# Optimization experiments

Hardware: AMD Instinct MI355X
Metric: run time of the kernel (lower is better)

Reference implementation:

```python
import jax, jax.numpy as jnp
import numpy as np

G, B, N, D = 3, 4096, 32, 256
C, H, A, L = 128, 8, 128, 16


def setup_inputs() -> dict:
    key = jax.random.key(0)
    ks = jax.random.split(key, 9)
    return {
        "targets": jax.random.normal(ks[0], (B, D), jnp.float32),
        "contexts": jax.random.normal(ks[1], (G, B, N, D), jnp.float32),
        "kernel": jax.random.normal(ks[2], (D, C), jnp.float32) * 0.05,
        "attn_kernel": jax.random.normal(ks[3], (1, H, 2 * C), jnp.float32) * 0.05,
        "attn_bias": jnp.zeros((H * C,), jnp.float32),
        "sem_kernel": jax.random.normal(ks[4], (H * C, A), jnp.float32) * 0.05,
        "sem_att_kernel": jax.random.normal(ks[5], (A, 1), jnp.float32) * 0.05,
        "dense_w": jax.random.normal(ks[6], (H * C, L), jnp.float32) * 0.05,
        "dense_b": jnp.zeros((L,), jnp.float32),
    }


def reference(targets, contexts, kernel, attn_kernel, attn_bias, sem_kernel,
              sem_att_kernel, dense_w, dense_b):
    # NodeAttention (shared weights across metapath groups; vectorized over G)
    node = jnp.einsum('bd,dc->bc', targets, kernel)            # [B,C]
    neigh = jnp.einsum('gbnd,dc->gbnc', contexts, kernel)      # [G,B,N,C]
    g, b, n, c = neigh.shape
    ak = attn_kernel[0]                                        # [H,2C]
    ak_node, ak_neigh = ak[:, :c], ak[:, c:]                   # split of concat([node, neigh])
    # scores[g,b,n,h] = concat(node_b, neigh_gbn) . ak_h
    scores = (jnp.einsum('bc,hc->bh', node, ak_node)[None, :, None, :]
              + jnp.einsum('gbnc,hc->gbnh', neigh, ak_neigh))  # [G,B,N,H]
    scores = jnp.transpose(scores, (0, 1, 3, 2))               # [G,B,H,N]
    coef = jax.nn.softmax(jax.nn.leaky_relu(scores, 0.2), axis=-1)
    z = jnp.einsum('gbhn,gbnc->gbhc', coef, neigh)             # [G,B,H,C]
    z = z.reshape(g, b, -1) + attn_bias                        # [G,B,H*C] (concat=True)
    # SemanticAttention over metapath groups
    inp = jnp.transpose(z, (1, 0, 2))                          # [B,G,HC]
    s = jnp.squeeze(jnp.matmul(jnp.tanh(jnp.matmul(inp, sem_kernel)), sem_att_kernel), -1)  # [B,G]
    att = jax.nn.softmax(s, axis=-1)
    pooled = jnp.einsum('bg,bgd->bd', att, inp)                # [B,HC]
    logits = pooled @ dense_w + dense_b                        # [B,L]
    return logits
```

## Files before the change

kernel.cpp:

```cpp
#include <hip/hip_runtime.h>
#include <hip/hip_bf16.h>

typedef float v4f __attribute__((ext_vector_type(4)));
typedef short v8s __attribute__((ext_vector_type(8)));

__device__ __forceinline__ unsigned short f2bf(float x){
    unsigned u = __float_as_uint(x);
    u += 0x7FFFu + ((u >> 16) & 1u);
    return (unsigned short)(u >> 16);
}
__device__ __forceinline__ float bf2f(unsigned short h){
    return __uint_as_float(((unsigned)h) << 16);
}
__device__ __forceinline__ v8s pack_bf8(v4f a, v4f b){
    union { v8s s; __hip_bfloat162 h[4]; } u;
    u.h[0] = __float22bfloat162_rn(float2{a[0],a[1]});
    u.h[1] = __float22bfloat162_rn(float2{a[2],a[3]});
    u.h[2] = __float22bfloat162_rn(float2{b[0],b[1]});
    u.h[3] = __float22bfloat162_rn(float2{b[2],b[3]});
    return u.s;
}

__global__ __launch_bounds__(256) void prep_all(const float* __restrict__ targ,
        const float* __restrict__ kern, const float* __restrict__ ak,
        const float* __restrict__ semk, float* __restrict__ ns,
        unsigned short* __restrict__ packB, unsigned short* __restrict__ pack2){
    __shared__ float wsh[256*8];
    int blk = blockIdx.x, t = threadIdx.x;
    if (blk < 16){
        {
            float a[8];
            #pragma unroll
            for (int h=0;h<8;h++) a[h]=0.f;
            const float* kr = kern + t*128;
            for (int c=0;c<128;c++){
                float kv = kr[c];
                #pragma unroll
                for (int h=0;h<8;h++) a[h] = fmaf(kv, ak[h*256+c], a[h]);
            }
            #pragma unroll
            for (int h=0;h<8;h++) wsh[t*8+h]=a[h];
        }
        __syncthreads();
        int b = blk*256 + t;
        float acc[8];
        #pragma unroll
        for (int h=0;h<8;h++) acc[h]=0.f;
        const float* tr = targ + (size_t)b*256;
        for (int d=0;d<256;d++){
            float tv = tr[d];
            #pragma unroll
            for (int h=0;h<8;h++) acc[h] = fmaf(tv, wsh[d*8+h], acc[h]);
        }
        #pragma unroll
        for (int h=0;h<8;h++) ns[b*8+h]=acc[h];
    } else if (blk < 18){
        {
            float a[8];
            #pragma unroll
            for (int h=0;h<8;h++) a[h]=0.f;
            const float* kr = kern + t*128;
            for (int c=0;c<128;c++){
                float kv = kr[c];
                #pragma unroll
                for (int h=0;h<8;h++) a[h] = fmaf(kv, ak[h*256+128+c], a[h]);
            }
            #pragma unroll
            for (int h=0;h<8;h++) wsh[t*8+h]=a[h];
        }
        __syncthreads();
        int gt = (blk-16)*256 + t;
        for (int r=0;r<72;r++){
            int e = gt + r*512;
            int j = e & 7; int l = (e>>3) & 63;
            int fc = e >> 9; int cc = fc % 9; int kk = fc / 9;
            int d = kk*32 + (l>>4)*8 + j;
            int c = cc*16 + (l&15);
            float v;
            if (cc < 8) v = kern[d*128 + c];
            else { int h = c - 128; v = (h < 8) ? wsh[d*8+h] : 0.0f; }
            packB[e] = f2bf(v);
        }
    } else {
        int gt = (blk-18)*256 + t;
        for (int r=0;r<16;r++){
            int e = gt + r*8192;
            int j = e & 7; int l = (e>>3) & 63;
            int cc = (e>>9) & 7; int gkk = e >> 12;
            int k = gkk*32 + (l>>4)*8 + j;
            int a2 = cc*16 + (l&15);
            pack2[e] = f2bf(semk[k*128 + a2]);
        }
    }
}

__global__ __launch_bounds__(256,4) void phase1(const float* __restrict__ ctx,
        const unsigned short* __restrict__ packB, const float* __restrict__ ns,
        const float* __restrict__ bias, unsigned short* __restrict__ zb16){
    __shared__ __align__(16) unsigned short outT[64*146];
    __shared__ float cf[2*32*8];

    int t = threadIdx.x;
    int bid = blockIdx.x;
    int g  = bid >> 11;
    int b0 = (bid & 2047) * 2;
    int w = t >> 6, lane = t & 63;

    const float* abase = ctx + (size_t)((g*4096 + b0)*32 + w*16 + (lane&15))*256 + ((lane>>4)*8);
    const unsigned short* bbase = packB + lane*8;

    v4f acc[9];
    #pragma unroll
    for (int i=0;i<9;i++) acc[i] = (v4f){0.f,0.f,0.f,0.f};

    #pragma unroll
    for (int kk=0;kk<8;kk++){
        v4f a0 = *(const v4f*)(abase + kk*32);
        v4f a1 = *(const v4f*)(abase + kk*32 + 4);
        v8s afr = pack_bf8(a0, a1);
        #pragma unroll
        for (int cc=0;cc<9;cc++){
            v8s bfr = *(const v8s*)(bbase + (kk*9+cc)*512);
            acc[cc] = __builtin_amdgcn_mfma_f32_16x16x32_bf16(afr, bfr, acc[cc], 0,0,0);
        }
    }

    int qr = (lane>>4)*4;
    #pragma unroll
    for (int cc=0;cc<9;cc++){
        int col = cc*16 + (lane&15);
        #pragma unroll
        for (int r=0;r<4;r++)
            outT[(w*16 + qr + r)*146 + col] = f2bf(acc[cc][r]);
    }
    __syncthreads();

    {
        int p = t >> 4, i = t & 15;
        int b = p >> 3, h = p & 7;
        float nsv = ns[(b0 + b)*8 + h];
        int row0 = b*32 + i, row1 = row0 + 16;
        float s0 = bf2f(outT[row0*146 + 128 + h]) + nsv;
        float s1 = bf2f(outT[row1*146 + 128 + h]) + nsv;
        s0 = s0 > 0.f ? s0 : 0.2f*s0;
        s1 = s1 > 0.f ? s1 : 0.2f*s1;
        float m = fmaxf(s0, s1);
        #pragma unroll
        for (int d=1; d<16; d<<=1) m = fmaxf(m, __shfl_xor(m, d));
        float e0 = __expf(s0 - m), e1 = __expf(s1 - m);
        float ssum = e0 + e1;
        #pragma unroll
        for (int d=1; d<16; d<<=1) ssum += __shfl_xor(ssum, d);
        float inv = 1.0f / ssum;
        cf[(b*32 + i)*8 + h]      = e0 * inv;
        cf[(b*32 + i + 16)*8 + h] = e1 * inv;
    }
    __syncthreads();

    {
        int b = t >> 7, c = t & 127;
        float az[8];
        #pragma unroll
        for (int h=0;h<8;h++) az[h]=0.f;
        for (int n=0;n<32;n++){
            float v = bf2f(outT[(b*32+n)*146 + c]);
            v4f c0 = *(const v4f*)&cf[(b*32+n)*8];
            v4f c1 = *(const v4f*)&cf[(b*32+n)*8 + 4];
            az[0] = fmaf(c0[0], v, az[0]); az[1] = fmaf(c0[1], v, az[1]);
            az[2] = fmaf(c0[2], v, az[2]); az[3] = fmaf(c0[3], v, az[3]);
            az[4] = fmaf(c1[0], v, az[4]); az[5] = fmaf(c1[1], v, az[5]);
            az[6] = fmaf(c1[2], v, az[6]); az[7] = fmaf(c1[3], v, az[7]);
        }
        size_t zb = ((size_t)(b0 + b)*3 + g)*1024;
        #pragma unroll
        for (int h=0;h<8;h++) zb16[zb + h*128 + c] = f2bf(az[h] + bias[h*128 + c]);
    }
}

__global__ __launch_bounds__(256) void semk2(const unsigned short* __restrict__ zb16,
        const unsigned short* __restrict__ pack2, const float* __restrict__ sa,
        float* __restrict__ sws){
    __shared__ float red[16*4];
    int t = threadIdx.x, w = t>>6, lane = t&63;
    int r0 = blockIdx.x * 16;
    v4f acc0 = (v4f){0.f,0.f,0.f,0.f};
    v4f acc1 = (v4f){0.f,0.f,0.f,0.f};
    const unsigned short* abase = zb16 + (size_t)(r0 + (lane&15))*1024 + (lane>>4)*8;
    #pragma unroll 4
    for (int kk=0; kk<32; kk++){
        v8s afr = *(const v8s*)(abase + kk*32);
        v8s b0  = *(const v8s*)(pack2 + (((kk*8 + w  )*64 + lane) << 3));
        v8s b1  = *(const v8s*)(pack2 + (((kk*8 + w+4)*64 + lane) << 3));
        acc0 = __builtin_amdgcn_mfma_f32_16x16x32_bf16(afr, b0, acc0, 0,0,0);
        acc1 = __builtin_amdgcn_mfma_f32_16x16x32_bf16(afr, b1, acc1, 0,0,0);
    }
    float sa0 = sa[w*16 + (lane&15)];
    float sa1 = sa[(w+4)*16 + (lane&15)];
    #pragma unroll
    for (int r=0;r<4;r++){
        float v = fmaf(tanhf(acc0[r]), sa0, tanhf(acc1[r]) * sa1);
        #pragma unroll
        for (int d=1; d<16; d<<=1) v += __shfl_xor(v, d);
        if ((lane&15)==0) red[((lane>>4)*4 + r)*4 + w] = v;
    }
    __syncthreads();
    if (t < 16)
        sws[r0 + t] = red[t*4] + red[t*4+1] + red[t*4+2] + red[t*4+3];
}

__global__ __launch_bounds__(64) void final3(const unsigned short* __restrict__ zb16,
        const float* __restrict__ sws, const float* __restrict__ dw,
        const float* __restrict__ db, float* __restrict__ outp){
    int b = blockIdx.x;
    int lane = threadIdx.x;
    float s0 = sws[b*3], s1 = sws[b*3+1], s2 = sws[b*3+2];
    float m = fmaxf(s0, fmaxf(s1, s2));
    float e0 = __expf(s0-m), e1 = __expf(s1-m), e2 = __expf(s2-m);
    float inv = 1.0f/(e0+e1+e2);
    float a0 = e0*inv, a1 = e1*inv, a2 = e2*inv;

    const unsigned short* z0 = zb16 + (size_t)b*3072 + lane*16;
    v8s za0 = *(const v8s*)(z0);          v8s za1 = *(const v8s*)(z0+8);
    v8s zb0 = *(const v8s*)(z0+1024);     v8s zb1 = *(const v8s*)(z0+1032);
    v8s zc0 = *(const v8s*)(z0+2048);     v8s zc1 = *(const v8s*)(z0+2056);
    float p[16];
    #pragma unroll
    for (int k=0;k<8;k++){
        p[k]   = a0*bf2f((unsigned short)za0[k]) + a1*bf2f((unsigned short)zb0[k]) + a2*bf2f((unsigned short)zc0[k]);
        p[k+8] = a0*bf2f((unsigned short)za1[k]) + a1*bf2f((unsigned short)zb1[k]) + a2*bf2f((unsigned short)zc1[k]);
    }
    float acc[16];
    #pragma unroll
    for (int l=0;l<16;l++) acc[l]=0.f;
    #pragma unroll
    for (int k=0;k<16;k++){
        const float* dr = dw + (lane*16 + k)*16;
        v4f d0 = *(const v4f*)(dr);
        v4f d1 = *(const v4f*)(dr+4);
        v4f d2 = *(const v4f*)(dr+8);
        v4f d3 = *(const v4f*)(dr+12);
        float pk = p[k];
        acc[0]=fmaf(pk,d0[0],acc[0]);  acc[1]=fmaf(pk,d0[1],acc[1]);
        acc[2]=fmaf(pk,d0[2],acc[2]);  acc[3]=fmaf(pk,d0[3],acc[3]);
        acc[4]=fmaf(pk,d1[0],acc[4]);  acc[5]=fmaf(pk,d1[1],acc[5]);
        acc[6]=fmaf(pk,d1[2],acc[6]);  acc[7]=fmaf(pk,d1[3],acc[7]);
        acc[8]=fmaf(pk,d2[0],acc[8]);  acc[9]=fmaf(pk,d2[1],acc[9]);
        acc[10]=fmaf(pk,d2[2],acc[10]); acc[11]=fmaf(pk,d2[3],acc[11]);
        acc[12]=fmaf(pk,d3[0],acc[12]); acc[13]=fmaf(pk,d3[1],acc[13]);
        acc[14]=fmaf(pk,d3[2],acc[14]); acc[15]=fmaf(pk,d3[3],acc[15]);
    }
    #pragma unroll
    for (int l=0;l<16;l++){
        float v = acc[l];
        #pragma unroll
        for (int d=1; d<64; d<<=1) v += __shfl_xor(v, d);
        acc[l] = v;
    }
    float myv = 0.f;
    #pragma unroll
    for (int l=0;l<16;l++) myv = (lane==l) ? acc[l] : myv;
    if (lane < 16) outp[b*16 + lane] = myv + db[lane];
}

extern "C" void kernel_launch(void* const* d_in, const int* in_sizes, int n_in,
                              void* d_out, int out_size, void* d_ws, size_t ws_size,
                              hipStream_t stream) {
    const float* targets  = (const float*)d_in[0];
    const float* contexts = (const float*)d_in[1];
    const float* kern     = (const float*)d_in[2];
    const float* ak       = (const float*)d_in[3];
    const float* bias     = (const float*)d_in[4];
    const float* semk     = (const float*)d_in[5];
    const float* sa       = (const float*)d_in[6];
    const float* dw       = (const float*)d_in[7];
    const float* db       = (const float*)d_in[8];
    float* outp = (float*)d_out;

    char* ws = (char*)d_ws;
    unsigned short* packB = (unsigned short*)(ws);
    float* nsb            = (float*)(ws + 73728);
    unsigned short* pack2 = (unsigned short*)(ws + 204800);
    unsigned short* zb16  = (unsigned short*)(ws + 466944);
    float* sws            = (float*)(ws + 25632768);

    prep_all<<<50, 256, 0, stream>>>(targets, kern, ak, semk, nsb, packB, pack2);
    phase1<<<6144, 256, 0, stream>>>(contexts, packB, nsb, bias, zb16);
    semk2<<<768, 256, 0, stream>>>(zb16, pack2, sa, sws);
    final3<<<4096, 64, 0, stream>>>(zb16, sws, dw, db, outp);
}
```

Baseline: 218.9 us.

## Make phase1 persistent with register double-buffered prefetch of context tiles

phase1 becomes a persistent kernel with 512 blocks, each looping over 12 tiles. While it runs the MFMA and attention math for the current tile, it prefetches the next tile's fp32 context fragments into a second register buffer. The LDS staging buffer now holds fp32 values instead of bf16, which removes a rounding step and enlarges shared memory. The costs are higher register pressure (launch bounds drop to 2 blocks per CU) and less parallelism for the latency hiding that many independent blocks used to provide.

```diff
diff --git a/kernel.cpp b/kernel.cpp
--- a/kernel.cpp
+++ b/kernel.cpp
@@ -94,86 +94,99 @@
     }
 }
 
-__global__ __launch_bounds__(256,4) void phase1(const float* __restrict__ ctx,
+#define P1_LOADA(BUF, TL) {                                                   \
+    int g_ = (TL) >> 11, bp_ = (TL) & 2047;                                   \
+    const float* ab_ = ctx + (size_t)(((g_*4096 + bp_*2)*32) + w*16 + arow)*256 + acol; \
+    _Pragma("unroll")                                                         \
+    for (int kk=0;kk<8;kk++){                                                 \
+        BUF[2*kk]   = *(const v4f*)(ab_ + kk*32);                             \
+        BUF[2*kk+1] = *(const v4f*)(ab_ + kk*32 + 4);                         \
+    } }
+
+#define P1_PROCESS(CUR, NXT, IT) {                                            \
+    int tl_ = tile0 + (IT);                                                   \
+    int pre_ = tile0 + (((IT)+1 < 12) ? (IT)+1 : 11);                         \
+    P1_LOADA(NXT, pre_);        \
+    v4f acc[9];                                                               \
+    _Pragma("unroll")                                                         \
+    for (int i=0;i<9;i++) acc[i] = (v4f){0.f,0.f,0.f,0.f};                    \
+    _Pragma("unroll")                                                         \
+    for (int kk=0;kk<8;kk++){                                                 \
+        v8s afr = pack_bf8(CUR[2*kk], CUR[2*kk+1]);                           \
+        _Pragma("unroll")                                                     \
+        for (int cc=0;cc<9;cc++){                                             \
+            v8s bfr = *(const v8s*)(bbase + (kk*9+cc)*512);                   \
+            acc[cc] = __builtin_amdgcn_mfma_f32_16x16x32_bf16(afr, bfr, acc[cc], 0,0,0); \
+        }                                                                     \
+    }                                                                         \
+    __syncthreads();           \
+    {   int qr = (lane>>4)*4;                                                 \
+        _Pragma("unroll")                                                     \
+        for (int cc=0;cc<9;cc++){                                             \
+            int col = cc*16 + (lane&15);                                      \
+            _Pragma("unroll")                                                 \
+            for (int r=0;r<4;r++)                                             \
+                outT[(w*16 + qr + r)*148 + col] = acc[cc][r];                 \
+        }                                                                     \
+    }                                                                         \
+    __syncthreads();                                                          \
+    int g_ = tl_ >> 11, b0_ = (tl_ & 2047)*2;                                 \
+    {   int p = t >> 4, i = t & 15;                                           \
+        int b = p >> 3, h = p & 7;                                            \
+        float nsv = ns[(b0_ + b)*8 + h];                                      \
+        float s0 = outT[(b*32+i)*148 + 128 + h] + nsv;                        \
+        float s1 = outT[(b*32+i+16)*148 + 128 + h] + nsv;                     \
+        s0 = s0 > 0.f ? s0 : 0.2f*s0;                                         \
+        s1 = s1 > 0.f ? s1 : 0.2f*s1;                                         \
+        float mx = fmaxf(s0, s1);                                             \
+        _Pragma("unroll")                                                     \
+        for (int d=1; d<16; d<<=1) mx = fmaxf(mx, __shfl_xor(mx, d));         \
+        float e0 = __expf(s0 - mx), e1 = __expf(s1 - mx);                     \
+        float ssum = e0 + e1;                                                 \
+        _Pragma("unroll")                                                     \
+        for (int d=1; d<16; d<<=1) ssum += __shfl_xor(ssum, d);               \
+        float inv = 1.0f / ssum;                                              \
+        cf[(b*32 + i)*8 + h]      = e0 * inv;                                 \
+        cf[(b*32 + i + 16)*8 + h] = e1 * inv;                                 \
+    }                                                                         \
+    __syncthreads();                                                          \
+    {   int b = t >> 7, c = t & 127;                                          \
+        float az[8];                                                          \
+        _Pragma("unroll")                                                     \
+        for (int h=0;h<8;h++) az[h]=0.f;                                      \
+        for (int n=0;n<32;n++){                                               \
+            float v = outT[(b*32+n)*148 + c];                                 \
+            v4f c0 = *(const v4f*)&cf[(b*32+n)*8];                            \
+            v4f c1 = *(const v4f*)&cf[(b*32+n)*8 + 4];                        \
+            az[0] = fmaf(c0[0], v, az[0]); az[1] = fmaf(c0[1], v, az[1]);     \
+            az[2] = fmaf(c0[2], v, az[2]); az[3] = fmaf(c0[3], v, az[3]);     \
+            az[4] = fmaf(c1[0], v, az[4]); az[5] = fmaf(c1[1], v, az[5]);     \
+            az[6] = fmaf(c1[2], v, az[6]); az[7] = fmaf(c1[3], v, az[7]);     \
+        }                                                                     \
+        size_t zb = ((size_t)(b0_ + b)*3 + g_)*1024;                          \
+        _Pragma("unroll")                                                     \
+        for (int h=0;h<8;h++) zb16[zb + h*128 + c] = f2bf(az[h] + bias[h*128 + c]); \
+    } }
+
+__global__ __launch_bounds__(256,2) void phase1(const float* __restrict__ ctx,
         const unsigned short* __restrict__ packB, const float* __restrict__ ns,
         const float* __restrict__ bias, unsigned short* __restrict__ zb16){
-    __shared__ __align__(16) unsigned short outT[64*146];
+    __shared__ __align__(16) float outT[64*148];
     __shared__ float cf[2*32*8];
 
     int t = threadIdx.x;
-    int bid = blockIdx.x;
-    int g  = bid >> 11;
-    int b0 = (bid & 2047) * 2;
     int w = t >> 6, lane = t & 63;
-
-    const float* abase = ctx + (size_t)((g*4096 + b0)*32 + w*16 + (lane&15))*256 + ((lane>>4)*8);
+    int arow = lane & 15, acol = (lane>>4)*8;
     const unsigned short* bbase = packB + lane*8;
-
-    v4f acc[9];
-    #pragma unroll
-    for (int i=0;i<9;i++) acc[i] = (v4f){0.f,0.f,0.f,0.f};
-
-    #pragma unroll
-    for (int kk=0;kk<8;kk++){
-        v4f a0 = *(const v4f*)(abase + kk*32);
-        v4f a1 = *(const v4f*)(abase + kk*32 + 4);
-        v8s afr = pack_bf8(a0, a1);
-        #pragma unroll
-        for (int cc=0;cc<9;cc++){
-            v8s bfr = *(const v8s*)(bbase + (kk*9+cc)*512);
-            acc[cc] = __builtin_amdgcn_mfma_f32_16x16x32_bf16(afr, bfr, acc[cc], 0,0,0);
-        }
-    }
-
-    int qr = (lane>>4)*4;
-    #pragma unroll
-    for (int cc=0;cc<9;cc++){
-        int col = cc*16 + (lane&15);
-        #pragma unroll
-        for (int r=0;r<4;r++)
-            outT[(w*16 + qr + r)*146 + col] = f2bf(acc[cc][r]);
-    }
-    __syncthreads();
-
-    {
-        int p = t >> 4, i = t & 15;
-        int b = p >> 3, h = p & 7;
-        float nsv = ns[(b0 + b)*8 + h];
-        int row0 = b*32 + i, row1 = row0 + 16;
-        float s0 = bf2f(outT[row0*146 + 128 + h]) + nsv;
-        float s1 = bf2f(outT[row1*146 + 128 + h]) + nsv;
-        s0 = s0 > 0.f ? s0 : 0.2f*s0;
-        s1 = s1 > 0.f ? s1 : 0.2f*s1;
-        float m = fmaxf(s0, s1);
-        #pragma unroll
-        for (int d=1; d<16; d<<=1) m = fmaxf(m, __shfl_xor(m, d));
-        float e0 = __expf(s0 - m), e1 = __expf(s1 - m);
-        float ssum = e0 + e1;
-        #pragma unroll
-        for (int d=1; d<16; d<<=1) ssum += __shfl_xor(ssum, d);
-        float inv = 1.0f / ssum;
-        cf[(b*32 + i)*8 + h]      = e0 * inv;
-        cf[(b*32 + i + 16)*8 + h] = e1 * inv;
-    }
-    __syncthreads();
-
-    {
-        int b = t >> 7, c = t & 127;
-        float az[8];
-        #pragma unroll
-        for (int h=0;h<8;h++) az[h]=0.f;
-        for (int n=0;n<32;n++){
-            float v = bf2f(outT[(b*32+n)*146 + c]);
-            v4f c0 = *(const v4f*)&cf[(b*32+n)*8];
-            v4f c1 = *(const v4f*)&cf[(b*32+n)*8 + 4];
-            az[0] = fmaf(c0[0], v, az[0]); az[1] = fmaf(c0[1], v, az[1]);
-            az[2] = fmaf(c0[2], v, az[2]); az[3] = fmaf(c0[3], v, az[3]);
-            az[4] = fmaf(c1[0], v, az[4]); az[5] = fmaf(c1[1], v, az[5]);
-            az[6] = fmaf(c1[2], v, az[6]); az[7] = fmaf(c1[3], v, az[7]);
-        }
-        size_t zb = ((size_t)(b0 + b)*3 + g)*1024;
-        #pragma unroll
-        for (int h=0;h<8;h++) zb16[zb + h*128 + c] = f2bf(az[h] + bias[h*128 + c]);
+    int tile0 = blockIdx.x * 12;
+
+    v4f A0[16], A1[16];
+    P1_LOADA(A0, tile0);
+
+    #pragma unroll 1
+    for (int it=0; it<12; it+=2){
+        P1_PROCESS(A0, A1, it);
+        P1_PROCESS(A1, A0, it+1);
     }
 }
 
@@ -284,7 +297,7 @@
     float* sws            = (float*)(ws + 25632768);
 
     prep_all<<<50, 256, 0, stream>>>(targets, kern, ak, semk, nsb, packB, pack2);
-    phase1<<<6144, 256, 0, stream>>>(contexts, packB, nsb, bias, zb16);
+    phase1<<<512, 256, 0, stream>>>(contexts, packB, nsb, bias, zb16);
     semk2<<<768, 256, 0, stream>>>(zb16, pack2, sa, sws);
     final3<<<4096, 64, 0, stream>>>(zb16, sws, dw, db, outp);
 }
```

Measured after the change: 402.2 us. +83.7%, slower.

## Give each wavefront a whole (g,b) row in phase1 and drop block barriers

Applied to the files above, without the earlier changes.

phase1 now assigns one full (group, batch) item of 32 neighbours to each wavefront. Each wavefront computes two 16-row MFMA tiles, does the per-head softmax in registers with cross-lane shuffles, and uses its own XOR-swizzled LDS slice, so the block-wide __syncthreads are gone. The weighted sum now handles two channels per lane and writes packed 32-bit bf16 pairs. This removes block synchronisation and LDS bank conflicts, but doubles the accumulator registers and lowers the occupancy hint from 4 to 2.

```diff
diff --git a/kernel.cpp b/kernel.cpp
--- a/kernel.cpp
+++ b/kernel.cpp
@@ -94,86 +94,104 @@
     }
 }
 
-__global__ __launch_bounds__(256,4) void phase1(const float* __restrict__ ctx,
+__global__ __launch_bounds__(256,2) void phase1(const float* __restrict__ ctx,
         const unsigned short* __restrict__ packB, const float* __restrict__ ns,
         const float* __restrict__ bias, unsigned short* __restrict__ zb16){
-    __shared__ __align__(16) unsigned short outT[64*146];
-    __shared__ float cf[2*32*8];
-
-    int t = threadIdx.x;
-    int bid = blockIdx.x;
-    int g  = bid >> 11;
-    int b0 = (bid & 2047) * 2;
-    int w = t >> 6, lane = t & 63;
-
-    const float* abase = ctx + (size_t)((g*4096 + b0)*32 + w*16 + (lane&15))*256 + ((lane>>4)*8);
+    __shared__ __align__(16) unsigned short outT[4][32*128];
+    __shared__ float cf[4][32*8];
+
+    int t = threadIdx.x, w = t >> 6, lane = t & 63;
+    int wt = blockIdx.x*4 + w;
+    int g = wt >> 12, b = wt & 4095;
+    int q = lane >> 4, h = lane & 15;
+
+    const float* ab = ctx + ((size_t)((g*4096 + b)*32) + h)*256 + q*8;
     const unsigned short* bbase = packB + lane*8;
 
-    v4f acc[9];
-    #pragma unroll
-    for (int i=0;i<9;i++) acc[i] = (v4f){0.f,0.f,0.f,0.f};
+    v4f acc0[9], acc1[9];
+    #pragma unroll
+    for (int i=0;i<9;i++){ acc0[i] = (v4f){0.f,0.f,0.f,0.f}; acc1[i] = (v4f){0.f,0.f,0.f,0.f}; }
 
     #pragma unroll
     for (int kk=0;kk<8;kk++){
-        v4f a0 = *(const v4f*)(abase + kk*32);
-        v4f a1 = *(const v4f*)(abase + kk*32 + 4);
-        v8s afr = pack_bf8(a0, a1);
+        v8s a0 = pack_bf8(*(const v4f*)(ab + kk*32),        *(const v4f*)(ab + kk*32 + 4));
+        v8s a1 = pack_bf8(*(const v4f*)(ab + 4096 + kk*32), *(const v4f*)(ab + 4096 + kk*32 + 4));
         #pragma unroll
         for (int cc=0;cc<9;cc++){
-            v8s bfr = *(const v8s*)(bbase + (kk*9+cc)*512);
-            acc[cc] = __builtin_amdgcn_mfma_f32_16x16x32_bf16(afr, bfr, acc[cc], 0,0,0);
-        }
-    }
-
-    int qr = (lane>>4)*4;
-    #pragma unroll
-    for (int cc=0;cc<9;cc++){
-        int col = cc*16 + (lane&15);
-        #pragma unroll
-        for (int r=0;r<4;r++)
-            outT[(w*16 + qr + r)*146 + col] = f2bf(acc[cc][r]);
-    }
-    __syncthreads();
+            v8s bf = *(const v8s*)(bbase + (kk*9+cc)*512);
+            acc0[cc] = __builtin_amdgcn_mfma_f32_16x16x32_bf16(a0, bf, acc0[cc], 0,0,0);
+            acc1[cc] = __builtin_amdgcn_mfma_f32_16x16x32_bf16(a1, bf, acc1[cc], 0,0,0);
+        }
+    }
 
     {
-        int p = t >> 4, i = t & 15;
-        int b = p >> 3, h = p & 7;
-        float nsv = ns[(b0 + b)*8 + h];
-        int row0 = b*32 + i, row1 = row0 + 16;
-        float s0 = bf2f(outT[row0*146 + 128 + h]) + nsv;
-        float s1 = bf2f(outT[row1*146 + 128 + h]) + nsv;
-        s0 = s0 > 0.f ? s0 : 0.2f*s0;
-        s1 = s1 > 0.f ? s1 : 0.2f*s1;
-        float m = fmaxf(s0, s1);
-        #pragma unroll
-        for (int d=1; d<16; d<<=1) m = fmaxf(m, __shfl_xor(m, d));
-        float e0 = __expf(s0 - m), e1 = __expf(s1 - m);
-        float ssum = e0 + e1;
-        #pragma unroll
-        for (int d=1; d<16; d<<=1) ssum += __shfl_xor(ssum, d);
-        float inv = 1.0f / ssum;
-        cf[(b*32 + i)*8 + h]      = e0 * inv;
-        cf[(b*32 + i + 16)*8 + h] = e1 * inv;
-    }
-    __syncthreads();
+        float nsv = (h < 8) ? ns[b*8 + h] : 0.f;
+        float sc[8];
+        #pragma unroll
+        for (int r=0;r<4;r++){ sc[r] = acc0[8][r] + nsv; sc[4+r] = acc1[8][r] + nsv; }
+        #pragma unroll
+        for (int i=0;i<8;i++) sc[i] = sc[i] > 0.f ? sc[i] : 0.2f*sc[i];
+        float mx = sc[0];
+        #pragma unroll
+        for (int i=1;i<8;i++) mx = fmaxf(mx, sc[i]);
+        mx = fmaxf(mx, __shfl_xor(mx, 16));
+        mx = fmaxf(mx, __shfl_xor(mx, 32));
+        float e[8], sum = 0.f;
+        #pragma unroll
+        for (int i=0;i<8;i++){ e[i] = __expf(sc[i]-mx); sum += e[i]; }
+        sum += __shfl_xor(sum, 16);
+        sum += __shfl_xor(sum, 32);
+        float inv = 1.0f / sum;
+        if (h < 8){
+            #pragma unroll
+            for (int r=0;r<4;r++){
+                cf[w][(q*4+r)*8 + h]      = e[r]*inv;
+                cf[w][(16+q*4+r)*8 + h]   = e[4+r]*inv;
+            }
+        }
+    }
+
+    #pragma unroll
+    for (int cc=0;cc<8;cc++){
+        #pragma unroll
+        for (int r=0;r<4;r++){
+            int row0 = q*4+r, row1 = 16+q*4+r;
+            int byte0 = (row0*256 + (cc*16+h)*2) ^ ((row0&7)<<5);
+            int byte1 = (row1*256 + (cc*16+h)*2) ^ ((row1&7)<<5);
+            *(unsigned short*)((char*)outT[w] + byte0) = f2bf(acc0[cc][r]);
+            *(unsigned short*)((char*)outT[w] + byte1) = f2bf(acc1[cc][r]);
+        }
+    }
 
     {
-        int b = t >> 7, c = t & 127;
-        float az[8];
-        #pragma unroll
-        for (int h=0;h<8;h++) az[h]=0.f;
+        float az0[8], az1[8];
+        #pragma unroll
+        for (int i=0;i<8;i++){ az0[i]=0.f; az1[i]=0.f; }
         for (int n=0;n<32;n++){
-            float v = bf2f(outT[(b*32+n)*146 + c]);
-            v4f c0 = *(const v4f*)&cf[(b*32+n)*8];
-            v4f c1 = *(const v4f*)&cf[(b*32+n)*8 + 4];
-            az[0] = fmaf(c0[0], v, az[0]); az[1] = fmaf(c0[1], v, az[1]);
-            az[2] = fmaf(c0[2], v, az[2]); az[3] = fmaf(c0[3], v, az[3]);
-            az[4] = fmaf(c1[0], v, az[4]); az[5] = fmaf(c1[1], v, az[5]);
-            az[6] = fmaf(c1[2], v, az[6]); az[7] = fmaf(c1[3], v, az[7]);
-        }
-        size_t zb = ((size_t)(b0 + b)*3 + g)*1024;
-        #pragma unroll
-        for (int h=0;h<8;h++) zb16[zb + h*128 + c] = f2bf(az[h] + bias[h*128 + c]);
+            int byte = (n*256 + lane*4) ^ ((n&7)<<5);
+            unsigned v = *(const unsigned*)((const char*)outT[w] + byte);
+            float v0 = bf2f((unsigned short)(v & 0xffffu));
+            float v1 = bf2f((unsigned short)(v >> 16));
+            v4f c0 = *(const v4f*)&cf[w][n*8];
+            v4f c1 = *(const v4f*)&cf[w][n*8 + 4];
+            az0[0]=fmaf(c0[0],v0,az0[0]); az0[1]=fmaf(c0[1],v0,az0[1]);
+            az0[2]=fmaf(c0[2],v0,az0[2]); az0[3]=fmaf(c0[3],v0,az0[3]);
+            az0[4]=fmaf(c1[0],v0,az0[4]); az0[5]=fmaf(c1[1],v0,az0[5]);
+            az0[6]=fmaf(c1[2],v0,az0[6]); az0[7]=fmaf(c1[3],v0,az0[7]);
+            az1[0]=fmaf(c0[0],v1,az1[0]); az1[1]=fmaf(c0[1],v1,az1[1]);
+            az1[2]=fmaf(c0[2],v1,az1[2]); az1[3]=fmaf(c0[3],v1,az1[3]);
+            az1[4]=fmaf(c1[0],v1,az1[4]); az1[5]=fmaf(c1[1],v1,az1[5]);
+            az1[6]=fmaf(c1[2],v1,az1[6]); az1[7]=fmaf(c1[3],v1,az1[7]);
+        }
+        size_t zb = ((size_t)b*3 + g)*1024;
+        int c0i = 2*lane;
+        #pragma unroll
+        for (int hh=0;hh<8;hh++){
+            unsigned short p0 = f2bf(az0[hh] + bias[hh*128 + c0i]);
+            unsigned short p1 = f2bf(az1[hh] + bias[hh*128 + c0i + 1]);
+            unsigned pk = ((unsigned)p1 << 16) | (unsigned)p0;
+            *(unsigned*)(zb16 + zb + hh*128 + c0i) = pk;
+        }
     }
 }
 
@@ -284,7 +302,7 @@
     float* sws            = (float*)(ws + 25632768);
 
     prep_all<<<50, 256, 0, stream>>>(targets, kern, ak, semk, nsb, packB, pack2);
-    phase1<<<6144, 256, 0, stream>>>(contexts, packB, nsb, bias, zb16);
+    phase1<<<3072, 256, 0, stream>>>(contexts, packB, nsb, bias, zb16);
     semk2<<<768, 256, 0, stream>>>(zb16, pack2, sa, sws);
     final3<<<4096, 64, 0, stream>>>(zb16, sws, dw, db, outp);
 }
```

Measured after the change: 197.6 us. 1.11x faster.
